# Kernel optimization log

Measured on AMD Instinct MI355X. Metric: run time of the kernel, lower is better.

## Reference

```python
import jax, jax.numpy as jnp
import numpy as np

HEAD_DIM = 128
N_HEADS = 16
N_KV_HEADS = 4
N_REP = N_HEADS // N_KV_HEADS


def _rope(x, cos, sin):
    # x: [B, S, Hk, D]; cos/sin: [S, D/2]
    xr = x.reshape(*x.shape[:-1], -1, 2)
    x0, x1 = xr[..., 0], xr[..., 1]
    c = cos[None, :, None, :]
    s = sin[None, :, None, :]
    o0 = x0 * c - x1 * s
    o1 = x0 * s + x1 * c
    return jnp.stack([o0, o1], axis=-1).reshape(x.shape)


def setup_inputs() -> dict:
    key = jax.random.key(0)
    ks = jax.random.split(key, 7)
    B, S, DIM = 2, 1024, 2048
    KV_DIM = HEAD_DIM * N_KV_HEADS
    x = jax.random.normal(ks[0], (B, S, DIM), dtype=jnp.float32)
    # rotary angles like LLaMA: freqs = 1/10000^(2i/D)
    inv_freq = 1.0 / (10000.0 ** (np.arange(0, HEAD_DIM, 2, dtype=np.float32) / HEAD_DIM))
    ang = np.arange(S, dtype=np.float32)[:, None] * inv_freq[None, :]  # [S, D/2]
    theta_cos = jnp.asarray(np.cos(ang))
    theta_sin = jnp.asarray(np.sin(ang))
    sc = 0.02
    wq = jax.random.normal(ks[1], (DIM, DIM), dtype=jnp.float32) * sc
    wk = jax.random.normal(ks[2], (DIM, KV_DIM), dtype=jnp.float32) * sc
    wv = jax.random.normal(ks[3], (DIM, KV_DIM), dtype=jnp.float32) * sc
    wo = jax.random.normal(ks[4], (DIM, DIM), dtype=jnp.float32) * sc
    return {"x": x, "theta_cos": theta_cos, "theta_sin": theta_sin,
            "wq": wq, "wk": wk, "wv": wv, "wo": wo}


def reference(x, theta_cos, theta_sin, wq, wk, wv, wo):
    B, S, DIM = x.shape
    # projections
    xq = (x @ wq).reshape(B, S, N_HEADS, HEAD_DIM).transpose(0, 2, 1, 3)  # [B,H,S,D]
    xk = (x @ wk).reshape(B, S, N_KV_HEADS, HEAD_DIM)                      # [B,S,Hk,D]
    xv = (x @ wv).reshape(B, S, N_KV_HEADS, HEAD_DIM)
    # RoPE on K and V only (faithful to source: Q is NOT rotated)
    xk = _rope(xk, theta_cos, theta_sin)
    xv = _rope(xv, theta_cos, theta_sin)
    # GQA repeat: [B,S,Hk,D] -> [B,H,S,D] (each kv head repeated consecutively)
    xk = jnp.repeat(xk.transpose(0, 2, 1, 3), N_REP, axis=1)
    xv = jnp.repeat(xv.transpose(0, 2, 1, 3), N_REP, axis=1)
    scale = HEAD_DIM ** (-0.5)
    att = jnp.einsum('bhqd,bhkd->bhqk', xq, xk) * scale
    # faithful masking: tril then masked_fill(att == 0, -inf)
    tri = jnp.tril(jnp.ones((S, S), dtype=bool))
    att = jnp.where(tri[None, None], att, 0.0)
    att = jnp.where(att == 0.0, -jnp.inf, att)
    att = jax.nn.softmax(att, axis=-1)
    y = jnp.einsum('bhqk,bhkd->bhqd', att, xv)
    out = y.transpose(0, 2, 1, 3).reshape(B, S, DIM)
    return out @ wo
```

## Files before the change

kernel.cpp:

```cpp
#include <hip/hip_runtime.h>
#include <hip/hip_bf16.h>
#include <stdint.h>

typedef _Float16 half_t;
typedef __attribute__((ext_vector_type(2))) _Float16 h2_t;
typedef __attribute__((ext_vector_type(4))) _Float16 h4_t;
typedef __attribute__((ext_vector_type(8))) _Float16 h8_t;
typedef __attribute__((ext_vector_type(4))) float f32x4;

__device__ __forceinline__ void gload16(const void* g, void* l) {
    __builtin_amdgcn_global_load_lds(
        (const __attribute__((address_space(1))) uint32_t*)(uintptr_t)g,
        (__attribute__((address_space(3))) uint32_t*)(uint32_t)(uintptr_t)l,
        16, 0, 0);
}

__global__ __launch_bounds__(256) void prep(const float* __restrict__ x, half_t* __restrict__ xh,
                                            const float* __restrict__ wq, const float* __restrict__ wk,
                                            const float* __restrict__ wv, const float* __restrict__ wo,
                                            half_t* __restrict__ qt, half_t* __restrict__ kt,
                                            half_t* __restrict__ vt, half_t* __restrict__ ot) {
    __shared__ half_t T[32][36];
    const int bx = blockIdx.x;
    if (bx < 2048) {
        int g = (bx * 256 + threadIdx.x) * 8;
        float4 a = *(const float4*)(x + g);
        float4 b = *(const float4*)(x + g + 4);
        h8_t o = {(half_t)a.x,(half_t)a.y,(half_t)a.z,(half_t)a.w,
                  (half_t)b.x,(half_t)b.y,(half_t)b.z,(half_t)b.w};
        *(h8_t*)(xh + g) = o;
        return;
    }
    const int wb = bx - 2048;
    const float* src; half_t* dst; int Nd, t;
    if (wb < 4096)      { src = wq; dst = qt; Nd = 2048; t = wb; }
    else if (wb < 5120) { src = wk; dst = kt; Nd = 512;  t = wb - 4096; }
    else if (wb < 6144) { src = wv; dst = vt; Nd = 512;  t = wb - 5120; }
    else                { src = wo; dst = ot; Nd = 2048; t = wb - 6144; }
    const int K = 2048;
    int nt = Nd >> 5;
    int ti = t / nt, tj = t % nt;
    int r  = threadIdx.x >> 3;
    int c4 = (threadIdx.x & 7) << 2;
    float4 v = *(const float4*)(src + (size_t)(ti*32 + r) * Nd + tj*32 + c4);
    T[r][c4+0] = (half_t)v.x; T[r][c4+1] = (half_t)v.y;
    T[r][c4+2] = (half_t)v.z; T[r][c4+3] = (half_t)v.w;
    __syncthreads();
    h4_t o = {T[c4+0][r], T[c4+1][r], T[c4+2][r], T[c4+3][r]};
    *(h4_t*)(dst + (size_t)(tj*32 + r) * K + ti*32 + c4) = o;
}

template<int BM, int QKV, typename CT>
__global__ __launch_bounds__(256) void gemm_t(const half_t* __restrict__ A,
                                              const half_t* __restrict__ Bq,
                                              const half_t* __restrict__ Bk,
                                              const half_t* __restrict__ Bv,
                                              CT* __restrict__ Cq,
                                              half_t* __restrict__ Ck,
                                              half_t* __restrict__ Cv,
                                              int NB, int K) {
    constexpr int MI  = BM / 32;
    constexpr int ACH = BM / 8;
    constexpr int TOT = ACH + 16;
    constexpr int PW  = TOT / 4;
    __shared__ half_t Ah[BM * 64];
    __shared__ half_t Bh[128 * 64];
    const int tid = threadIdx.x, lane = tid & 63, wid = tid >> 6;
    const int lr = lane & 15, lg = lane >> 4;
    const int wm = wid >> 1, wn = wid & 1;
    const int nwg = gridDim.x, bid = blockIdx.x;
    const int swz = (bid & 7) * (nwg >> 3) + (bid >> 3);
    const int bm = swz / NB, bn = swz % NB;
    const int m0 = bm * BM;

    const half_t* W; CT* Cc; int cs, col0;
    if constexpr (QKV) {
        if (bn < 16)      { W = Bq + (size_t)bn * 128 * K;        Cc = Cq;       cs = 2048; col0 = bn * 128; }
        else if (bn < 20) { W = Bk + (size_t)(bn - 16) * 128 * K; Cc = (CT*)Ck;  cs = 512;  col0 = (bn - 16) * 128; }
        else              { W = Bv + (size_t)(bn - 20) * 128 * K; Cc = (CT*)Cv;  cs = 512;  col0 = (bn - 20) * 128; }
    } else {
        W = Bq + (size_t)bn * 128 * K; Cc = Cq; cs = NB * 128; col0 = bn * 128;
    }

    const half_t* Arow = A + (size_t)m0 * K;
    f32x4 acc[MI][4] = {};

    for (int k0 = 0; k0 < K; k0 += 64) {
        #pragma unroll
        for (int c = 0; c < PW; c++) {
            const int chunk = wid * PW + c;
            const int o = lane * 16;
            if (chunk < ACH) {
                const int go   = (chunk << 10) + o;
                const int row  = go >> 7;
                const int colb = (go & 127) ^ ((row & 7) << 4);
                gload16(Arow + (size_t)row * K + k0 + (colb >> 1), (char*)Ah + (chunk << 10));
            } else {
                const int go   = ((chunk - ACH) << 10) + o;
                const int row  = go >> 7;
                const int colb = (go & 127) ^ ((row & 7) << 4);
                gload16(W + (size_t)row * K + k0 + (colb >> 1), (char*)Bh + ((chunk - ACH) << 10));
            }
        }
        __syncthreads();
        h8_t af[2][MI], bf[2][4];
        #pragma unroll
        for (int kk = 0; kk < 2; kk++) {
            #pragma unroll
            for (int mi = 0; mi < MI; mi++) {
                const int row = wm * (BM / 2) + mi * 16 + lr;
                const int cb  = (kk * 64 + lg * 16) ^ ((lr & 7) << 4);
                af[kk][mi] = *(const h8_t*)((const char*)Ah + row * 128 + cb);
            }
            #pragma unroll
            for (int ni = 0; ni < 4; ni++) {
                const int row = wn * 64 + ni * 16 + lr;
                const int cb  = (kk * 64 + lg * 16) ^ ((lr & 7) << 4);
                bf[kk][ni] = *(const h8_t*)((const char*)Bh + row * 128 + cb);
            }
        }
        #pragma unroll
        for (int kk = 0; kk < 2; kk++)
            #pragma unroll
            for (int mi = 0; mi < MI; mi++)
                #pragma unroll
                for (int ni = 0; ni < 4; ni++)
                    acc[mi][ni] = __builtin_amdgcn_mfma_f32_16x16x32_f16(af[kk][mi], bf[kk][ni], acc[mi][ni], 0, 0, 0);
        __syncthreads();
    }

    #pragma unroll
    for (int mi = 0; mi < MI; mi++)
        #pragma unroll
        for (int ni = 0; ni < 4; ni++)
            #pragma unroll
            for (int r = 0; r < 4; r++) {
                int row = m0 + wm * (BM / 2) + mi * 16 + lg * 4 + r;
                int col = col0 + wn * 64 + ni * 16 + lr;
                Cc[(size_t)row * cs + col] = (CT)acc[mi][ni][r];
            }
}

__global__ __launch_bounds__(256) void rope(half_t* __restrict__ Kh, const half_t* __restrict__ Vh,
                                            half_t* __restrict__ Vt, const float* __restrict__ cs,
                                            const float* __restrict__ sn) {
    const int bx = blockIdx.x;
    if (bx < 2048) {
        int gid = bx * 256 + threadIdx.x;
        int row = gid >> 8;
        int pc  = gid & 255;
        int s   = row & 1023;
        int p   = pc & 63;
        float c = cs[s * 64 + p], si = sn[s * 64 + p];
        h2_t v = *(h2_t*)(Kh + (size_t)row * 512 + 2 * pc);
        float x0 = (float)v[0], x1 = (float)v[1];
        h2_t o = {(half_t)(x0 * c - x1 * si), (half_t)(x0 * si + x1 * c)};
        *(h2_t*)(Kh + (size_t)row * 512 + 2 * pc) = o;
        return;
    }
    int gid = (bx - 2048) * 256 + threadIdx.x;
    int col = gid & 2047;
    int dp  = gid >> 11;
    int s   = col & 1023;
    int p   = dp & 63;
    float c = cs[s * 64 + p], si = sn[s * 64 + p];
    h2_t v = *(const h2_t*)(Vh + (size_t)col * 512 + 2 * dp);
    float x0 = (float)v[0], x1 = (float)v[1];
    Vt[(size_t)(2 * dp)     * 2048 + col] = (half_t)(x0 * c - x1 * si);
    Vt[(size_t)(2 * dp + 1) * 2048 + col] = (half_t)(x0 * si + x1 * c);
}

__global__ __launch_bounds__(256) void attn3(const half_t* __restrict__ Qh, const half_t* __restrict__ Kh,
                                             const half_t* __restrict__ Vt, half_t* __restrict__ Yh) {
    __shared__ half_t Ktile[64 * 128];
    __shared__ half_t Vtile[128 * 64];
    __shared__ half_t Pl[4][16][72];

    const int tid = threadIdx.x, lane = tid & 63, wid = tid >> 6;
    const int lr = lane & 15, lg = lane >> 4;
    const int bx = blockIdx.x;
    const int g  = bx & 7;
    const int local = bx >> 3;
    const int b = g >> 2, kvh = g & 3;
    const int h = kvh * 4 + (local & 3);
    const int qt = 15 - (local >> 2);
    const int nkb = qt + 1;
    const int qbase = qt * 64 + wid * 16;
    const size_t qrow0 = (size_t)(b * 1024 + qbase);
    const size_t kbase = (size_t)b * 1024;

    const float sc = 0.08838834764831845f;
    h8_t qf[4];
    #pragma unroll
    for (int kk = 0; kk < 4; kk++) {
        qf[kk] = *(const h8_t*)(Qh + (qrow0 + lr) * 2048 + h * 128 + kk * 32 + lg * 8);
        qf[kk] = qf[kk] * (half_t)sc;
    }

    float m[4], l[4];
    f32x4 yacc[8] = {};
    #pragma unroll
    for (int r = 0; r < 4; r++) { m[r] = -1e30f; l[r] = 0.f; }

    for (int kb = 0; kb < nkb; kb++) {
        const int j = kb * 64;
        __syncthreads();
        #pragma unroll
        for (int c = 0; c < 4; c++) {
            const int chunk = wid * 4 + c;
            const int o = (chunk << 10) + lane * 16;
            { const int row  = o >> 8;
              const int colb = (o & 255) ^ ((row & 7) << 4);
              gload16(Kh + (kbase + j + row) * 512 + kvh * 128 + (colb >> 1),
                      (char*)Ktile + (chunk << 10)); }
            { const int row  = o >> 7;
              const int colb = (o & 127) ^ ((row & 7) << 4);
              gload16(Vt + (size_t)(kvh * 128 + row) * 2048 + kbase + j + (colb >> 1),
                      (char*)Vtile + (chunk << 10)); }
        }
        __syncthreads();

        f32x4 st[4] = {};
        #pragma unroll
        for (int t = 0; t < 4; t++)
            #pragma unroll
            for (int kk = 0; kk < 4; kk++) {
                const int row = t * 16 + lr;
                const int cb  = (kk * 64 + lg * 16) ^ ((lr & 7) << 4);
                h8_t kf = *(const h8_t*)((const char*)Ktile + row * 256 + cb);
                st[t] = __builtin_amdgcn_mfma_f32_16x16x32_f16(qf[kk], kf, st[t], 0, 0, 0);
            }
        if (kb == nkb - 1) {
            #pragma unroll
            for (int t = 0; t < 4; t++)
                #pragma unroll
                for (int r = 0; r < 4; r++) {
                    int q = qbase + lg * 4 + r;
                    if (j + t * 16 + lr > q) st[t][r] = -1e30f;
                }
        }
        float mb[4];
        #pragma unroll
        for (int r = 0; r < 4; r++)
            mb[r] = fmaxf(fmaxf(st[0][r], st[1][r]), fmaxf(st[2][r], st[3][r]));
        #pragma unroll
        for (int off = 1; off < 16; off <<= 1)
            #pragma unroll
            for (int r = 0; r < 4; r++)
                mb[r] = fmaxf(mb[r], __shfl_xor(mb[r], off));
        float al[4];
        #pragma unroll
        for (int r = 0; r < 4; r++) {
            float mn = fmaxf(m[r], mb[r]);
            al[r] = __expf(m[r] - mn);
            m[r]  = mn;
        }
        float rs[4] = {0.f, 0.f, 0.f, 0.f};
        #pragma unroll
        for (int t = 0; t < 4; t++)
            #pragma unroll
            for (int r = 0; r < 4; r++) {
                float p = __expf(st[t][r] - m[r]);
                st[t][r] = p;
                rs[r] += p;
            }
        #pragma unroll
        for (int off = 1; off < 16; off <<= 1)
            #pragma unroll
            for (int r = 0; r < 4; r++)
                rs[r] += __shfl_xor(rs[r], off);
        #pragma unroll
        for (int r = 0; r < 4; r++) l[r] = l[r] * al[r] + rs[r];
        #pragma unroll
        for (int dt = 0; dt < 8; dt++)
            #pragma unroll
            for (int r = 0; r < 4; r++)
                yacc[dt][r] *= al[r];
        #pragma unroll
        for (int t = 0; t < 4; t++)
            #pragma unroll
            for (int r = 0; r < 4; r++)
                Pl[wid][lg * 4 + r][t * 16 + lr] = (half_t)st[t][r];
        h8_t pa0 = *(const h8_t*)(&Pl[wid][lr][lg * 8]);
        h8_t pa1 = *(const h8_t*)(&Pl[wid][lr][32 + lg * 8]);
        #pragma unroll
        for (int dt = 0; dt < 8; dt++) {
            const int row = dt * 16 + lr;
            const int cb0 = (lg * 16) ^ ((lr & 7) << 4);
            const int cb1 = (64 + lg * 16) ^ ((lr & 7) << 4);
            h8_t v0 = *(const h8_t*)((const char*)Vtile + row * 128 + cb0);
            h8_t v1 = *(const h8_t*)((const char*)Vtile + row * 128 + cb1);
            yacc[dt] = __builtin_amdgcn_mfma_f32_16x16x32_f16(pa0, v0, yacc[dt], 0, 0, 0);
            yacc[dt] = __builtin_amdgcn_mfma_f32_16x16x32_f16(pa1, v1, yacc[dt], 0, 0, 0);
        }
    }

    #pragma unroll
    for (int r = 0; r < 4; r++) l[r] = 1.0f / l[r];
    #pragma unroll
    for (int dt = 0; dt < 8; dt++)
        #pragma unroll
        for (int r = 0; r < 4; r++)
            Yh[(qrow0 + lg * 4 + r) * 2048 + h * 128 + dt * 16 + lr] = (half_t)(yacc[dt][r] * l[r]);
}

extern "C" void kernel_launch(void* const* d_in, const int* in_sizes, int n_in,
                              void* d_out, int out_size, void* d_ws, size_t ws_size,
                              hipStream_t stream) {
    const float* x  = (const float*)d_in[0];
    const float* tc = (const float*)d_in[1];
    const float* ts = (const float*)d_in[2];
    const float* wq = (const float*)d_in[3];
    const float* wk = (const float*)d_in[4];
    const float* wv = (const float*)d_in[5];
    const float* wo = (const float*)d_in[6];
    float* out = (float*)d_out;

    const size_t MD = 2048ull * 2048, MK = 2048ull * 512;
    half_t* Xh  = (half_t*)d_ws;
    half_t* Qh  = Xh  + MD;
    half_t* Kh  = Qh  + MD;
    half_t* Vh  = Kh  + MK;
    half_t* Vt  = Vh  + MK;
    half_t* Yh  = Vt  + MK;
    half_t* wqt = Yh  + MD;
    half_t* wkt = wqt + MD;
    half_t* wvt = wkt + MK;
    half_t* wot = wvt + MK;

    prep<<<12288, 256, 0, stream>>>(x, Xh, wq, wk, wv, wo, wqt, wkt, wvt, wot);
    gemm_t<64, 1, half_t><<<768, 256, 0, stream>>>(Xh, wqt, wkt, wvt, Qh, Kh, Vh, 24, 2048);
    rope<<<4096, 256, 0, stream>>>(Kh, Vh, Vt, tc, ts);
    attn3<<<512, 256, 0, stream>>>(Qh, Kh, Vt, Yh);
    gemm_t<64, 0, float><<<512, 256, 0, stream>>>(Yh, wot, nullptr, nullptr, out, nullptr, nullptr, 16, 2048);
}
```

Before: 126.5 us.

## Double-buffer K/V tiles in attention and reorder query tiles

The attention kernel now keeps two LDS buffers each for K and V. It issues the async global-to-LDS loads for the next key block before computing on the current one, so the load waits at the top of each iteration can overlap with MFMA work. The query-tile order changes from strictly descending to the eight heaviest tiles followed by the lightest tiles in ascending order, which aims for better load balance across the causal workload. In exchange, LDS use per block roughly doubles, which may lower occupancy.

```diff
diff --git a/kernel.cpp b/kernel.cpp
--- a/kernel.cpp
+++ b/kernel.cpp
@@ -170,10 +170,10 @@
     Vt[(size_t)(2 * dp + 1) * 2048 + col] = (half_t)(x0 * si + x1 * c);
 }
 
-__global__ __launch_bounds__(256) void attn3(const half_t* __restrict__ Qh, const half_t* __restrict__ Kh,
-                                             const half_t* __restrict__ Vt, half_t* __restrict__ Yh) {
-    __shared__ half_t Ktile[64 * 128];
-    __shared__ half_t Vtile[128 * 64];
+__global__ __launch_bounds__(256) void attn4(const half_t* __restrict__ Qh, const half_t* __restrict__ Kh,
+                                             const half_t* __restrict__ Vtg, half_t* __restrict__ Yh) {
+    __shared__ half_t K0[64 * 128], K1[64 * 128];
+    __shared__ half_t V0[128 * 64], V1[128 * 64];
     __shared__ half_t Pl[4][16][72];
 
     const int tid = threadIdx.x, lane = tid & 63, wid = tid >> 6;
@@ -183,7 +183,8 @@
     const int local = bx >> 3;
     const int b = g >> 2, kvh = g & 3;
     const int h = kvh * 4 + (local & 3);
-    const int qt = 15 - (local >> 2);
+    const int li = local >> 2;
+    const int qt = (li < 8) ? (15 - li) : (li - 8);
     const int nkb = qt + 1;
     const int qbase = qt * 64 + wid * 16;
     const size_t qrow0 = (size_t)(b * 1024 + qbase);
@@ -202,9 +203,8 @@
     #pragma unroll
     for (int r = 0; r < 4; r++) { m[r] = -1e30f; l[r] = 0.f; }
 
-    for (int kb = 0; kb < nkb; kb++) {
+    auto stage = [&](half_t* kt, half_t* vb, int kb) {
         const int j = kb * 64;
-        __syncthreads();
         #pragma unroll
         for (int c = 0; c < 4; c++) {
             const int chunk = wid * 4 + c;
@@ -212,14 +212,16 @@
             { const int row  = o >> 8;
               const int colb = (o & 255) ^ ((row & 7) << 4);
               gload16(Kh + (kbase + j + row) * 512 + kvh * 128 + (colb >> 1),
-                      (char*)Ktile + (chunk << 10)); }
+                      (char*)kt + (chunk << 10)); }
             { const int row  = o >> 7;
               const int colb = (o & 127) ^ ((row & 7) << 4);
-              gload16(Vt + (size_t)(kvh * 128 + row) * 2048 + kbase + j + (colb >> 1),
-                      (char*)Vtile + (chunk << 10)); }
-        }
-        __syncthreads();
-
+              gload16(Vtg + (size_t)(kvh * 128 + row) * 2048 + kbase + j + (colb >> 1),
+                      (char*)vb + (chunk << 10)); }
+        }
+    };
+
+    auto iter = [&](const half_t* kt, const half_t* vb, int kb) {
+        const int j = kb * 64;
         f32x4 st[4] = {};
         #pragma unroll
         for (int t = 0; t < 4; t++)
@@ -227,7 +229,7 @@
             for (int kk = 0; kk < 4; kk++) {
                 const int row = t * 16 + lr;
                 const int cb  = (kk * 64 + lg * 16) ^ ((lr & 7) << 4);
-                h8_t kf = *(const h8_t*)((const char*)Ktile + row * 256 + cb);
+                h8_t kf = *(const h8_t*)((const char*)kt + row * 256 + cb);
                 st[t] = __builtin_amdgcn_mfma_f32_16x16x32_f16(qf[kk], kf, st[t], 0, 0, 0);
             }
         if (kb == nkb - 1) {
@@ -288,10 +290,23 @@
             const int row = dt * 16 + lr;
             const int cb0 = (lg * 16) ^ ((lr & 7) << 4);
             const int cb1 = (64 + lg * 16) ^ ((lr & 7) << 4);
-            h8_t v0 = *(const h8_t*)((const char*)Vtile + row * 128 + cb0);
-            h8_t v1 = *(const h8_t*)((const char*)Vtile + row * 128 + cb1);
+            h8_t v0 = *(const h8_t*)((const char*)vb + row * 128 + cb0);
+            h8_t v1 = *(const h8_t*)((const char*)vb + row * 128 + cb1);
             yacc[dt] = __builtin_amdgcn_mfma_f32_16x16x32_f16(pa0, v0, yacc[dt], 0, 0, 0);
             yacc[dt] = __builtin_amdgcn_mfma_f32_16x16x32_f16(pa1, v1, yacc[dt], 0, 0, 0);
+        }
+    };
+
+    stage(K0, V0, 0);
+    __syncthreads();
+    for (int kb = 0; kb < nkb; kb += 2) {
+        if (kb + 1 < nkb) stage(K1, V1, kb + 1);
+        iter(K0, V0, kb);
+        __syncthreads();
+        if (kb + 1 < nkb) {
+            if (kb + 2 < nkb) stage(K0, V0, kb + 2);
+            iter(K1, V1, kb + 1);
+            __syncthreads();
         }
     }
 
@@ -331,6 +346,6 @@
     prep<<<12288, 256, 0, stream>>>(x, Xh, wq, wk, wv, wo, wqt, wkt, wvt, wot);
     gemm_t<64, 1, half_t><<<768, 256, 0, stream>>>(Xh, wqt, wkt, wvt, Qh, Kh, Vh, 24, 2048);
     rope<<<4096, 256, 0, stream>>>(Kh, Vh, Vt, tc, ts);
-    attn3<<<512, 256, 0, stream>>>(Qh, Kh, Vt, Yh);
+    attn4<<<512, 256, 0, stream>>>(Qh, Kh, Vt, Yh);
     gemm_t<64, 0, float><<<512, 256, 0, stream>>>(Yh, wot, nullptr, nullptr, out, nullptr, nullptr, 16, 2048);
 }
```

After: 122.5 us. 3.2% less time.

## Split long causal query tiles across two blocks with merge kernel, exp2 softmax, lazy rescale

Applied to the files above, without the earlier changes.

Query tiles 8-15 are each split into two key-range halves processed by separate blocks, which write unnormalized partial outputs plus row max/sum to workspace; a new merge kernel combines them. This balances the triangular causal workload across 768 blocks instead of 512 uneven ones. The softmax now uses exp2 with log2e folded into the Q scale, and skips the rescale of the accumulator when the running max grows by no more than 8, which relies on FP32 headroom. The cost is an extra kernel launch and extra FP32 partial-result traffic.

```diff
diff --git a/kernel.cpp b/kernel.cpp
--- a/kernel.cpp
+++ b/kernel.cpp
@@ -1,12 +1,19 @@
 #include <hip/hip_runtime.h>
 #include <hip/hip_bf16.h>
 #include <stdint.h>
+#include <math.h>
 
 typedef _Float16 half_t;
 typedef __attribute__((ext_vector_type(2))) _Float16 h2_t;
 typedef __attribute__((ext_vector_type(4))) _Float16 h4_t;
 typedef __attribute__((ext_vector_type(8))) _Float16 h8_t;
 typedef __attribute__((ext_vector_type(4))) float f32x4;
+
+#if __has_builtin(__builtin_amdgcn_exp2f)
+#define EXP2(x) __builtin_amdgcn_exp2f(x)
+#else
+#define EXP2(x) exp2f(x)
+#endif
 
 __device__ __forceinline__ void gload16(const void* g, void* l) {
     __builtin_amdgcn_global_load_lds(
@@ -170,10 +177,14 @@
     Vt[(size_t)(2 * dp + 1) * 2048 + col] = (half_t)(x0 * si + x1 * c);
 }
 
-__global__ __launch_bounds__(256) void attn3(const half_t* __restrict__ Qh, const half_t* __restrict__ Kh,
-                                             const half_t* __restrict__ Vt, half_t* __restrict__ Yh) {
-    __shared__ half_t Ktile[64 * 128];
-    __shared__ half_t Vtile[128 * 64];
+__global__ __launch_bounds__(256, 3) void attn6(const half_t* __restrict__ Qh,
+                                                const half_t* __restrict__ Kh,
+                                                const half_t* __restrict__ Vtg,
+                                                half_t* __restrict__ Yh,
+                                                float* __restrict__ Yp,
+                                                float* __restrict__ ML) {
+    __shared__ half_t K0[64 * 128];
+    __shared__ half_t V0[128 * 64];
     __shared__ half_t Pl[4][16][72];
 
     const int tid = threadIdx.x, lane = tid & 63, wid = tid >> 6;
@@ -183,18 +194,22 @@
     const int local = bx >> 3;
     const int b = g >> 2, kvh = g & 3;
     const int h = kvh * 4 + (local & 3);
-    const int qt = 15 - (local >> 2);
-    const int nkb = qt + 1;
+    const int piece = local >> 2;
+    int qt, kb0, kb1, part; bool partial;
+    if (piece < 8)       { qt = piece;      kb0 = 0; kb1 = qt; partial = false; part = 0; }
+    else if (piece < 16) { qt = piece;      kb0 = 0; kb1 = 7;  partial = true;  part = 0; }
+    else                 { qt = piece - 8;  kb0 = 8; kb1 = qt; partial = true;  part = 1; }
+
     const int qbase = qt * 64 + wid * 16;
     const size_t qrow0 = (size_t)(b * 1024 + qbase);
     const size_t kbase = (size_t)b * 1024;
 
-    const float sc = 0.08838834764831845f;
+    const float sc2 = 0.08838834764831845f * 1.4426950408889634f;
     h8_t qf[4];
     #pragma unroll
     for (int kk = 0; kk < 4; kk++) {
         qf[kk] = *(const h8_t*)(Qh + (qrow0 + lr) * 2048 + h * 128 + kk * 32 + lg * 8);
-        qf[kk] = qf[kk] * (half_t)sc;
+        qf[kk] = qf[kk] * (half_t)sc2;
     }
 
     float m[4], l[4];
@@ -202,7 +217,7 @@
     #pragma unroll
     for (int r = 0; r < 4; r++) { m[r] = -1e30f; l[r] = 0.f; }
 
-    for (int kb = 0; kb < nkb; kb++) {
+    for (int kb = kb0; kb <= kb1; kb++) {
         const int j = kb * 64;
         __syncthreads();
         #pragma unroll
@@ -212,31 +227,31 @@
             { const int row  = o >> 8;
               const int colb = (o & 255) ^ ((row & 7) << 4);
               gload16(Kh + (kbase + j + row) * 512 + kvh * 128 + (colb >> 1),
-                      (char*)Ktile + (chunk << 10)); }
+                      (char*)K0 + (chunk << 10)); }
             { const int row  = o >> 7;
               const int colb = (o & 127) ^ ((row & 7) << 4);
-              gload16(Vt + (size_t)(kvh * 128 + row) * 2048 + kbase + j + (colb >> 1),
-                      (char*)Vtile + (chunk << 10)); }
+              gload16(Vtg + (size_t)(kvh * 128 + row) * 2048 + kbase + j + (colb >> 1),
+                      (char*)V0 + (chunk << 10)); }
         }
         __syncthreads();
 
         f32x4 st[4] = {};
         #pragma unroll
-        for (int t = 0; t < 4; t++)
+        for (int t4 = 0; t4 < 4; t4++)
             #pragma unroll
             for (int kk = 0; kk < 4; kk++) {
-                const int row = t * 16 + lr;
+                const int row = t4 * 16 + lr;
                 const int cb  = (kk * 64 + lg * 16) ^ ((lr & 7) << 4);
-                h8_t kf = *(const h8_t*)((const char*)Ktile + row * 256 + cb);
-                st[t] = __builtin_amdgcn_mfma_f32_16x16x32_f16(qf[kk], kf, st[t], 0, 0, 0);
-            }
-        if (kb == nkb - 1) {
-            #pragma unroll
-            for (int t = 0; t < 4; t++)
+                h8_t kf = *(const h8_t*)((const char*)K0 + row * 256 + cb);
+                st[t4] = __builtin_amdgcn_mfma_f32_16x16x32_f16(qf[kk], kf, st[t4], 0, 0, 0);
+            }
+        if (kb == qt) {
+            #pragma unroll
+            for (int t4 = 0; t4 < 4; t4++)
                 #pragma unroll
                 for (int r = 0; r < 4; r++) {
                     int q = qbase + lg * 4 + r;
-                    if (j + t * 16 + lr > q) st[t][r] = -1e30f;
+                    if (j + t4 * 16 + lr > q) st[t4][r] = -1e30f;
                 }
         }
         float mb[4];
@@ -248,20 +263,31 @@
             #pragma unroll
             for (int r = 0; r < 4; r++)
                 mb[r] = fmaxf(mb[r], __shfl_xor(mb[r], off));
-        float al[4];
-        #pragma unroll
-        for (int r = 0; r < 4; r++) {
-            float mn = fmaxf(m[r], mb[r]);
-            al[r] = __expf(m[r] - mn);
-            m[r]  = mn;
+        float need = 0.f;
+        #pragma unroll
+        for (int r = 0; r < 4; r++) need = fmaxf(need, mb[r] - m[r]);
+        if (!__all(need <= 8.0f)) {
+            float al[4];
+            #pragma unroll
+            for (int r = 0; r < 4; r++) {
+                float mn = fmaxf(m[r], mb[r]);
+                al[r] = EXP2(m[r] - mn);
+                m[r]  = mn;
+                l[r] *= al[r];
+            }
+            #pragma unroll
+            for (int dt = 0; dt < 8; dt++)
+                #pragma unroll
+                for (int r = 0; r < 4; r++)
+                    yacc[dt][r] *= al[r];
         }
         float rs[4] = {0.f, 0.f, 0.f, 0.f};
         #pragma unroll
-        for (int t = 0; t < 4; t++)
+        for (int t4 = 0; t4 < 4; t4++)
             #pragma unroll
             for (int r = 0; r < 4; r++) {
-                float p = __expf(st[t][r] - m[r]);
-                st[t][r] = p;
+                float p = EXP2(st[t4][r] - m[r]);
+                st[t4][r] = p;
                 rs[r] += p;
             }
         #pragma unroll
@@ -270,17 +296,12 @@
             for (int r = 0; r < 4; r++)
                 rs[r] += __shfl_xor(rs[r], off);
         #pragma unroll
-        for (int r = 0; r < 4; r++) l[r] = l[r] * al[r] + rs[r];
-        #pragma unroll
-        for (int dt = 0; dt < 8; dt++)
+        for (int r = 0; r < 4; r++) l[r] += rs[r];
+        #pragma unroll
+        for (int t4 = 0; t4 < 4; t4++)
             #pragma unroll
             for (int r = 0; r < 4; r++)
-                yacc[dt][r] *= al[r];
-        #pragma unroll
-        for (int t = 0; t < 4; t++)
-            #pragma unroll
-            for (int r = 0; r < 4; r++)
-                Pl[wid][lg * 4 + r][t * 16 + lr] = (half_t)st[t][r];
+                Pl[wid][lg * 4 + r][t4 * 16 + lr] = (half_t)st[t4][r];
         h8_t pa0 = *(const h8_t*)(&Pl[wid][lr][lg * 8]);
         h8_t pa1 = *(const h8_t*)(&Pl[wid][lr][32 + lg * 8]);
         #pragma unroll
@@ -288,20 +309,75 @@
             const int row = dt * 16 + lr;
             const int cb0 = (lg * 16) ^ ((lr & 7) << 4);
             const int cb1 = (64 + lg * 16) ^ ((lr & 7) << 4);
-            h8_t v0 = *(const h8_t*)((const char*)Vtile + row * 128 + cb0);
-            h8_t v1 = *(const h8_t*)((const char*)Vtile + row * 128 + cb1);
+            h8_t v0 = *(const h8_t*)((const char*)V0 + row * 128 + cb0);
+            h8_t v1 = *(const h8_t*)((const char*)V0 + row * 128 + cb1);
             yacc[dt] = __builtin_amdgcn_mfma_f32_16x16x32_f16(pa0, v0, yacc[dt], 0, 0, 0);
             yacc[dt] = __builtin_amdgcn_mfma_f32_16x16x32_f16(pa1, v1, yacc[dt], 0, 0, 0);
         }
     }
 
+    if (!partial) {
+        #pragma unroll
+        for (int r = 0; r < 4; r++) {
+            float inv = 1.0f / l[r];
+            #pragma unroll
+            for (int dt = 0; dt < 8; dt++)
+                Yh[(qrow0 + lg * 4 + r) * 2048 + h * 128 + dt * 16 + lr] =
+                    (half_t)(yacc[dt][r] * inv);
+        }
+    } else {
+        const int pidx = ((b * 16 + h) * 8 + (qt - 8)) * 2 + part;
+        float* yp = Yp + (size_t)pidx * 8192;
+        #pragma unroll
+        for (int r = 0; r < 4; r++) {
+            const int rl = wid * 16 + lg * 4 + r;
+            #pragma unroll
+            for (int dt = 0; dt < 8; dt++)
+                yp[rl * 128 + dt * 16 + lr] = yacc[dt][r];
+        }
+        if (lr == 0) {
+            float* ml = ML + (size_t)pidx * 128;
+            #pragma unroll
+            for (int r = 0; r < 4; r++) {
+                const int rl = wid * 16 + lg * 4 + r;
+                ml[rl]      = m[r];
+                ml[64 + rl] = l[r];
+            }
+        }
+    }
+}
+
+__global__ __launch_bounds__(256) void merge(const float* __restrict__ Yp,
+                                             const float* __restrict__ ML,
+                                             half_t* __restrict__ Yh) {
+    const int sidx = blockIdx.x;
+    const int b = sidx >> 7;
+    const int rem = sidx & 127;
+    const int h = rem >> 3;
+    const int qt = 8 + (rem & 7);
+    const int t = threadIdx.x;
+    const int row = t >> 2;
+    const int cg = (t & 3) * 32;
+    const float* ml0 = ML + (size_t)(sidx * 2) * 128;
+    const float* ml1 = ml0 + 128;
+    const float m0 = ml0[row], l0 = ml0[64 + row];
+    const float m1 = ml1[row], l1 = ml1[64 + row];
+    const float M  = fmaxf(m0, m1);
+    const float w0 = EXP2(m0 - M), w1 = EXP2(m1 - M);
+    const float inv = 1.0f / (w0 * l0 + w1 * l1);
+    const float* y0 = Yp + (size_t)(sidx * 2) * 8192 + row * 128 + cg;
+    const float* y1 = y0 + 8192;
+    half_t* out = Yh + ((size_t)(b * 1024 + qt * 64 + row)) * 2048 + h * 128 + cg;
     #pragma unroll
-    for (int r = 0; r < 4; r++) l[r] = 1.0f / l[r];
-    #pragma unroll
-    for (int dt = 0; dt < 8; dt++)
-        #pragma unroll
-        for (int r = 0; r < 4; r++)
-            Yh[(qrow0 + lg * 4 + r) * 2048 + h * 128 + dt * 16 + lr] = (half_t)(yacc[dt][r] * l[r]);
+    for (int c = 0; c < 32; c += 4) {
+        float4 a = *(const float4*)(y0 + c);
+        float4 d = *(const float4*)(y1 + c);
+        h4_t o = {(half_t)((w0 * a.x + w1 * d.x) * inv),
+                  (half_t)((w0 * a.y + w1 * d.y) * inv),
+                  (half_t)((w0 * a.z + w1 * d.z) * inv),
+                  (half_t)((w0 * a.w + w1 * d.w) * inv)};
+        *(h4_t*)(out + c) = o;
+    }
 }
 
 extern "C" void kernel_launch(void* const* d_in, const int* in_sizes, int n_in,
@@ -327,10 +403,13 @@
     half_t* wkt = wqt + MD;
     half_t* wvt = wkt + MK;
     half_t* wot = wvt + MK;
+    float*  Yp  = (float*)(wot + MD);
+    float*  ML  = Yp + 512ull * 8192;
 
     prep<<<12288, 256, 0, stream>>>(x, Xh, wq, wk, wv, wo, wqt, wkt, wvt, wot);
     gemm_t<64, 1, half_t><<<768, 256, 0, stream>>>(Xh, wqt, wkt, wvt, Qh, Kh, Vh, 24, 2048);
     rope<<<4096, 256, 0, stream>>>(Kh, Vh, Vt, tc, ts);
-    attn3<<<512, 256, 0, stream>>>(Qh, Kh, Vt, Yh);
+    attn6<<<768, 256, 0, stream>>>(Qh, Kh, Vt, Yh, Yp, ML);
+    merge<<<256, 256, 0, stream>>>(Yp, ML, Yh);
     gemm_t<64, 0, float><<<512, 256, 0, stream>>>(Yh, wot, nullptr, nullptr, out, nullptr, nullptr, 16, 2048);
 }
```

Result: no change. 128.9 us (+1.9%).
